# Performance work log

Hardware: AMD Instinct MI355X
Metric: run time of the kernel (lower is better)

## Reference

```python
import jax, jax.numpy as jnp
import numpy as np

B, T, E, H = 4, 2048, 1024, 1024

def setup_inputs() -> dict:
    key = jax.random.key(0)
    k1, k2, k3, k4 = jax.random.split(key, 4)
    inputs = jax.random.normal(k1, (B, T, E), dtype=jnp.float32)
    # Dense(size, use_bias=False) -> weight [emb, size], glorot-ish scale
    Wq = jax.random.normal(k2, (E, H), dtype=jnp.float32) * (1.0 / np.sqrt(E))
    Wk = jax.random.normal(k3, (E, H), dtype=jnp.float32) * (1.0 / np.sqrt(E))
    Wv = jax.random.normal(k4, (E, H), dtype=jnp.float32) * (1.0 / np.sqrt(E))
    return {"inputs": inputs, "Wq": Wq, "Wk": Wk, "Wv": Wv}

def reference(inputs, Wq, Wk, Wv):
    # inputs: [B, T, E]
    _, Tc, Ec = inputs.shape
    q = inputs @ Wq  # [B, T, H]
    k = inputs @ Wk  # [B, T, H]
    v = inputs @ Wv  # [B, T, H]
    # scores scaled by emb_dim**-0.5 (NOT head size) as in the source
    w = jnp.einsum('bih,bjh->bij', q, k) * (Ec ** -0.5)  # [B, T, T]
    tril = jnp.tril(jnp.ones((Tc, Tc), dtype=bool))
    w = jnp.where(tril, w, -jnp.inf)
    # NOTE: source uses softmax over axis=1 (query axis), non-standard but faithful
    w = jax.nn.softmax(w, axis=1)
    # dropout_rate=0.0 -> identity
    out = w @ v  # [B, T, H]
    return out
```

## Files before the change

kernel.cpp:

```cpp
#include <hip/hip_runtime.h>
#include <hip/hip_bf16.h>
#include <stdint.h>


typedef short bf16x8 __attribute__((ext_vector_type(8)));
typedef float f32x4  __attribute__((ext_vector_type(4)));

__device__ __forceinline__ unsigned short f2bf(float f) {
    union { float f; unsigned u; } x; x.f = f;
    unsigned r = x.u + 0x7FFFu + ((x.u >> 16) & 1u);
    return (unsigned short)(r >> 16);
}
__device__ __forceinline__ float bf2f(unsigned short h) {
    union { unsigned u; float f; } x; x.u = ((unsigned)h) << 16;
    return x.f;
}

__global__ __launch_bounds__(256) void cast_kernel(
    const float* __restrict__ in, unsigned short* __restrict__ out, size_t n)
{
    size_t i = ((size_t)blockIdx.x * 256 + threadIdx.x) * 4;
    if (i >= n) return;
    float4 v = *(const float4*)(in + i);
    union { unsigned short h[4]; unsigned long long u; } p;
    p.h[0] = f2bf(v.x); p.h[1] = f2bf(v.y); p.h[2] = f2bf(v.z); p.h[3] = f2bf(v.w);
    *(unsigned long long*)(out + i) = p.u;
}

__global__ __launch_bounds__(256) void transpose_cast_kernel(
    const float* __restrict__ in, unsigned short* __restrict__ out, int R, int C)
{
    __shared__ unsigned short tile[64][65];
    int tx = threadIdx.x & 63, ty = threadIdx.x >> 6;
    int r0 = blockIdx.y * 64, c0 = blockIdx.x * 64;
#pragma unroll
    for (int i = 0; i < 16; ++i) {
        int r = ty + i * 4;
        tile[r][tx] = f2bf(in[(size_t)(r0 + r) * C + c0 + tx]);
    }
    __syncthreads();
#pragma unroll
    for (int i = 0; i < 16; ++i) {
        int c = ty + i * 4;
        out[(size_t)(c0 + c) * R + r0 + tx] = tile[tx][c];
    }
}

template <int MODE>
__global__ __launch_bounds__(256, 3) void gemm_nt(
    const unsigned short* __restrict__ A, const unsigned short* __restrict__ B,
    void* __restrict__ Cout, unsigned short* __restrict__ C2,
    unsigned short* __restrict__ C3, float* __restrict__ fpar,
    int M, int N, int K,
    size_t sAb, size_t sBb, size_t sCb, float scale, int ldt)
{
    int tn, tm, bz = blockIdx.z;
    if (MODE == 4) {
        unsigned id = blockIdx.y * gridDim.x + blockIdx.x;
        unsigned xcd = id & 7, k2 = id >> 3;
        tm = (int)(xcd * 8 + (k2 & 7));
        tn = (int)(k2 >> 3);
    } else if (MODE == 5) {
        int tid = blockIdx.x;
        tm = (int)((sqrtf(8.f * (float)tid + 1.f) - 1.f) * 0.5f);
        while ((tm + 1) * (tm + 2) / 2 <= tid) ++tm;
        while (tm * (tm + 1) / 2 > tid) --tm;
        tn = tid - tm * (tm + 1) / 2;
    } else {
        tn = blockIdx.x; tm = blockIdx.y;
    }
    A += (size_t)bz * sAb;
    B += (size_t)bz * sBb;
    int m0 = tm * 128, n0 = tn * 128;
    int kmax = (MODE == 2) ? (m0 + 128) : K;

    __shared__ unsigned short sAB[2 * 128 * 64];
    char* sAc = (char*)sAB;
    char* sBc = (char*)sAB + 16384;

    unsigned t = threadIdx.x, lane = t & 63, wave = t >> 6;

    unsigned srow = t >> 2;
    unsigned gsw = (t & 3) ^ ((t >> 3) & 3);
    const unsigned short* pA = A + (size_t)(m0 + srow) * K + gsw * 8;
    const unsigned short* pB = B + (size_t)(n0 + srow) * K + gsw * 8;
    const size_t rstep = (size_t)64 * K;
    unsigned ldsOff = t * 16;

    unsigned wm = (wave >> 1) * 64, wn = (wave & 1) * 64;
    unsigned lrow = lane & 15;
    unsigned lk = ((lane >> 4) ^ ((lane >> 1) & 3)) * 8;
    const short* sAs = (const short*)sAB;
    const short* sBs = (const short*)(sAB + 128 * 64);

    f32x4 acc[4][4] = {};

    int4 rA0 = *(const int4*)(pA);
    int4 rA1 = *(const int4*)(pA + rstep);
    int4 rA2 = *(const int4*)(pA + 32);
    int4 rA3 = *(const int4*)(pA + rstep + 32);
    int4 rB0 = *(const int4*)(pB);
    int4 rB1 = *(const int4*)(pB + rstep);
    int4 rB2 = *(const int4*)(pB + 32);
    int4 rB3 = *(const int4*)(pB + rstep + 32);

    for (int k0 = 0; k0 < kmax; k0 += 64) {
        __syncthreads();
        *(int4*)(sAc + ldsOff)         = rA0;
        *(int4*)(sAc + ldsOff + 4096)  = rA1;
        *(int4*)(sAc + ldsOff + 8192)  = rA2;
        *(int4*)(sAc + ldsOff + 12288) = rA3;
        *(int4*)(sBc + ldsOff)         = rB0;
        *(int4*)(sBc + ldsOff + 4096)  = rB1;
        *(int4*)(sBc + ldsOff + 8192)  = rB2;
        *(int4*)(sBc + ldsOff + 12288) = rB3;
        __syncthreads();

        if (k0 + 64 < kmax) {
            pA += 64; pB += 64;
            rA0 = *(const int4*)(pA);
            rA1 = *(const int4*)(pA + rstep);
            rA2 = *(const int4*)(pA + 32);
            rA3 = *(const int4*)(pA + rstep + 32);
            rB0 = *(const int4*)(pB);
            rB1 = *(const int4*)(pB + rstep);
            rB2 = *(const int4*)(pB + 32);
            rB3 = *(const int4*)(pB + rstep + 32);
        }

#pragma unroll
        for (int kk = 0; kk < 2; ++kk) {
            bf16x8 a[4], b[4];
#pragma unroll
            for (int i = 0; i < 4; ++i) {
                a[i] = *(const bf16x8*)(sAs + kk * 4096 + (wm + i * 16 + lrow) * 32 + lk);
                b[i] = *(const bf16x8*)(sBs + kk * 4096 + (wn + i * 16 + lrow) * 32 + lk);
            }
#pragma unroll
            for (int i = 0; i < 4; ++i)
#pragma unroll
                for (int j = 0; j < 4; ++j)
                    acc[i][j] = __builtin_amdgcn_mfma_f32_16x16x32_bf16(
                        a[i], b[j], acc[i][j], 0, 0, 0);
        }
    }

    unsigned col = lane & 15, rq = (lane >> 4) * 4;
    if (MODE == 2) {
        float* C = (float*)Cout + (size_t)bz * sCb;
#pragma unroll
        for (int i = 0; i < 4; ++i)
#pragma unroll
            for (int j = 0; j < 4; ++j)
#pragma unroll
                for (int r = 0; r < 4; ++r)
                    C[(size_t)(m0 + wm + i * 16 + rq + r) * N + n0 + wn + j * 16 + col] =
                        acc[i][j][r];
    } else if (MODE == 5) {
        unsigned short* Ebp = (unsigned short*)Cout + (size_t)bz * sCb;
        float* par = fpar + (size_t)bz * 32 * 2048;
        bool diag = (tm == tn);
        unsigned short* tile = sAB;
        __syncthreads();
#pragma unroll
        for (int jj = 0; jj < 4; ++jj) {
            float csum = 0.f;
            int jl = (int)(wn + jj * 16 + col);
            int jg = n0 + jl;
#pragma unroll
            for (int ii = 0; ii < 4; ++ii) {
#pragma unroll
                for (int r = 0; r < 4; ++r) {
                    int il = (int)(wm + ii * 16 + rq + r);
                    int ig = m0 + il;
                    unsigned short us = 0;
                    if (!diag || ig >= jg)
                        us = f2bf(__expf(acc[ii][jj][r] * scale));
                    tile[il * 128 + jl] = us;
                    csum += bf2f(us);
                }
            }
            csum += __shfl_xor(csum, 16);
            csum += __shfl_xor(csum, 32);
            if (lane < 16) {
                int rh = (m0 + wm) >> 6;
                par[(size_t)rh * 2048 + n0 + wn + jj * 16 + lane] = csum;
            }
        }
        __syncthreads();
        {
            unsigned rr = t >> 4, cc = (t & 15) * 8;
#pragma unroll
            for (int p = 0; p < 8; ++p) {
                int li = (int)(p * 16 + rr);
                int4 v = *(const int4*)(tile + li * 128 + cc);
                *(int4*)(Ebp + (size_t)(m0 + li) * N + n0 + cc) = v;
            }
        }
    } else {
        if (n0 < 2048) {
            unsigned short* C = (n0 < 1024) ? (unsigned short*)Cout : C2;
            int nb = n0 & 1023;
#pragma unroll
            for (int i = 0; i < 4; ++i)
#pragma unroll
                for (int j = 0; j < 4; ++j)
#pragma unroll
                    for (int r = 0; r < 4; ++r)
                        C[(size_t)(m0 + wm + i * 16 + rq + r) * 1024 + nb + wn + j * 16 + col] =
                            f2bf(acc[i][j][r]);
        } else {
            int batch = m0 >> 11, tb = m0 & 2047;
            unsigned short* C = C3 + (size_t)batch * 1024 * 2048;
#pragma unroll
            for (int i = 0; i < 4; ++i)
#pragma unroll
                for (int j = 0; j < 4; ++j) {
                    union { unsigned short h[4]; unsigned long long u; } p;
#pragma unroll
                    for (int r = 0; r < 4; ++r) p.h[r] = f2bf(acc[i][j][r]);
                    int h = (n0 - 2048) + wn + j * 16 + col;
                    int t0 = tb + wm + i * 16 + rq;
                    *(unsigned long long*)(C + (size_t)h * ldt + t0) = p.u;
                }
        }
    }
}

__global__ __launch_bounds__(256) void colsum_inv(
    const float* __restrict__ par, float* __restrict__ Linv, int T)
{
    int b = blockIdx.y;
    int j = blockIdx.x * 256 + threadIdx.x;
    const float* p = par + (size_t)b * 32 * 2048;
    float s = 0.f;
    for (int rh = j >> 6; rh < 32; ++rh) s += p[(size_t)rh * 2048 + j];
    Linv[b * 2048 + j] = 1.0f / s;
}

__global__ __launch_bounds__(256) void scale_v(
    unsigned short* __restrict__ Vt, const float* __restrict__ Linv)
{
    size_t idx = ((size_t)blockIdx.x * 256 + threadIdx.x) * 8;
    int b = (int)(idx >> 21);
    int tt = (int)(idx & 2047);
    bf16x8 v = *(bf16x8*)(Vt + idx);
    const float* L = Linv + b * 2048 + tt;
#pragma unroll
    for (int e = 0; e < 8; ++e)
        v[e] = (short)f2bf(bf2f((unsigned short)v[e]) * L[e]);
    *(bf16x8*)(Vt + idx) = v;
}

extern "C" void kernel_launch(void* const* d_in, const int* in_sizes, int n_in,
                              void* d_out, int out_size, void* d_ws, size_t ws_size,
                              hipStream_t stream)
{
    const int B = 4, T = 2048, E = 1024, H = 1024;
    const int M = B * T;
    const float* X  = (const float*)d_in[0];
    const float* Wq = (const float*)d_in[1];
    const float* Wk = (const float*)d_in[2];
    const float* Wv = (const float*)d_in[3];
    float* out = (float*)d_out;
    char* ws = (char*)d_ws;
    const size_t MB = 1024 * 1024;

    unsigned short* Xb  = (unsigned short*)(ws + 0);
    unsigned short* WqT = (unsigned short*)(ws + 16 * MB);
    unsigned short* WkT = (unsigned short*)(ws + 18 * MB);
    unsigned short* WvT = (unsigned short*)(ws + 20 * MB);
    unsigned short* Qb  = (unsigned short*)(ws + 32 * MB);
    unsigned short* Kb  = (unsigned short*)(ws + 48 * MB);
    unsigned short* Vt  = (unsigned short*)(ws + 64 * MB);
    unsigned short* Eb  = (unsigned short*)(ws + 0);
    float*          Linv = (float*)(ws + 32 * MB);
    float*          par  = (float*)d_out;

    cast_kernel<<<dim3((M * E) / 1024), 256, 0, stream>>>(X, Xb, (size_t)M * E);
    transpose_cast_kernel<<<dim3(H / 64, E / 64), 256, 0, stream>>>(Wq, WqT, E, H);
    transpose_cast_kernel<<<dim3(H / 64, E / 64), 256, 0, stream>>>(Wk, WkT, E, H);
    transpose_cast_kernel<<<dim3(H / 64, E / 64), 256, 0, stream>>>(Wv, WvT, E, H);

    gemm_nt<4><<<dim3(3 * H / 128, M / 128, 1), 256, 0, stream>>>(
        Xb, WqT, Qb, Kb, Vt, nullptr, M, 3 * H, E, 0, 0, 0, 1.f, T);

    gemm_nt<5><<<dim3(136, 1, B), 256, 0, stream>>>(
        Qb, Kb, Eb, nullptr, nullptr, par, T, T, H,
        (size_t)T * H, (size_t)T * H, (size_t)T * T, 0.03125f, T);

    colsum_inv<<<dim3(T / 256, B), 256, 0, stream>>>(par, Linv, T);
    scale_v<<<dim3((B * H * T) / 2048), 256, 0, stream>>>(Vt, Linv);

    gemm_nt<2><<<dim3(H / 128, T / 128, B), 256, 0, stream>>>(
        Eb, Vt, out, nullptr, nullptr, nullptr, T, H, T,
        (size_t)T * T, (size_t)H * T, (size_t)T * H, 1.f, 0);
}
```

Baseline: 251.6 us.

## Fuse prep kernels, fuse colsum with V scaling, remap GEMM block schedules

Merges the X cast and the three weight transpose-casts into one launch, and merges the column-sum/inverse with the V scaling so the inverse stays in shared memory. Block-to-tile mapping changes: the triangular QK^T grid is interleaved so blocks on the same XCD get a spread of tile workloads, and the causal PV GEMM runs as a flattened 1D grid that pairs heavy and light row tiles across batches. The aim is fewer launches and better load balance across XCDs. The cost is more complex index math, and the fused colsum_scale has only 128 blocks, which may underuse the GPU.

Result: faster. 228.4 us (-9.2%).

```diff
diff --git a/kernel.cpp b/kernel.cpp
--- a/kernel.cpp
+++ b/kernel.cpp
@@ -16,33 +16,41 @@
     return x.f;
 }
 
-__global__ __launch_bounds__(256) void cast_kernel(
-    const float* __restrict__ in, unsigned short* __restrict__ out, size_t n)
-{
-    size_t i = ((size_t)blockIdx.x * 256 + threadIdx.x) * 4;
-    if (i >= n) return;
-    float4 v = *(const float4*)(in + i);
-    union { unsigned short h[4]; unsigned long long u; } p;
-    p.h[0] = f2bf(v.x); p.h[1] = f2bf(v.y); p.h[2] = f2bf(v.z); p.h[3] = f2bf(v.w);
-    *(unsigned long long*)(out + i) = p.u;
-}
-
-__global__ __launch_bounds__(256) void transpose_cast_kernel(
-    const float* __restrict__ in, unsigned short* __restrict__ out, int R, int C)
+__global__ __launch_bounds__(256) void prep_kernel(
+    const float* __restrict__ X,
+    const float* __restrict__ Wq, const float* __restrict__ Wk,
+    const float* __restrict__ Wv,
+    unsigned short* __restrict__ Xb, unsigned short* __restrict__ WT)
 {
     __shared__ unsigned short tile[64][65];
-    int tx = threadIdx.x & 63, ty = threadIdx.x >> 6;
-    int r0 = blockIdx.y * 64, c0 = blockIdx.x * 64;
-#pragma unroll
-    for (int i = 0; i < 16; ++i) {
-        int r = ty + i * 4;
-        tile[r][tx] = f2bf(in[(size_t)(r0 + r) * C + c0 + tx]);
-    }
-    __syncthreads();
-#pragma unroll
-    for (int i = 0; i < 16; ++i) {
-        int c = ty + i * 4;
-        out[(size_t)(c0 + c) * R + r0 + tx] = tile[tx][c];
+    unsigned id = blockIdx.x;
+    if (id < 8192) {
+        size_t i = ((size_t)id * 256 + threadIdx.x) * 4;
+        float4 v = *(const float4*)(X + i);
+        union { unsigned short h[4]; unsigned long long u; } p;
+        p.h[0] = f2bf(v.x); p.h[1] = f2bf(v.y);
+        p.h[2] = f2bf(v.z); p.h[3] = f2bf(v.w);
+        *(unsigned long long*)(Xb + i) = p.u;
+    } else {
+        unsigned w = id - 8192;
+        unsigned which = w >> 8;
+        const float* W = (which == 0) ? Wq : (which == 1) ? Wk : Wv;
+        unsigned short* out = WT + (size_t)which * 1024 * 1024;
+        const int R = 1024, C = 1024;
+        unsigned t2 = w & 255;
+        int c0 = (int)(t2 & 15) * 64, r0 = (int)(t2 >> 4) * 64;
+        int tx = threadIdx.x & 63, ty = threadIdx.x >> 6;
+#pragma unroll
+        for (int i = 0; i < 16; ++i) {
+            int r = ty + i * 4;
+            tile[r][tx] = f2bf(W[(size_t)(r0 + r) * C + c0 + tx]);
+        }
+        __syncthreads();
+#pragma unroll
+        for (int i = 0; i < 16; ++i) {
+            int c = ty + i * 4;
+            out[(size_t)(c0 + c) * R + r0 + tx] = tile[tx][c];
+        }
     }
 }
 
@@ -61,13 +69,18 @@
         tm = (int)(xcd * 8 + (k2 & 7));
         tn = (int)(k2 >> 3);
     } else if (MODE == 5) {
-        int tid = blockIdx.x;
+        int bxr = blockIdx.x;
+        int tid = (bxr & 7) * 17 + (bxr >> 3);
         tm = (int)((sqrtf(8.f * (float)tid + 1.f) - 1.f) * 0.5f);
         while ((tm + 1) * (tm + 2) / 2 <= tid) ++tm;
         while (tm * (tm + 1) / 2 > tid) --tm;
         tn = tid - tm * (tm + 1) / 2;
     } else {
-        tn = blockIdx.x; tm = blockIdx.y;
+        unsigned n = blockIdx.x;
+        tn = (int)(n & 7u);
+        unsigned q = n >> 3, half = q >> 5, r = q & 31u;
+        bz = (int)((half ? 2u : 0u) + (r & 1u));
+        tm = half ? (int)(r >> 1) : (int)(15u - (r >> 1));
     }
     A += (size_t)bz * sAb;
     B += (size_t)bz * sBb;
@@ -227,29 +240,32 @@
     }
 }
 
-__global__ __launch_bounds__(256) void colsum_inv(
-    const float* __restrict__ par, float* __restrict__ Linv, int T)
+__global__ __launch_bounds__(256) void colsum_scale(
+    const float* __restrict__ par, unsigned short* __restrict__ Vt)
 {
-    int b = blockIdx.y;
-    int j = blockIdx.x * 256 + threadIdx.x;
-    const float* p = par + (size_t)b * 32 * 2048;
-    float s = 0.f;
-    for (int rh = j >> 6; rh < 32; ++rh) s += p[(size_t)rh * 2048 + j];
-    Linv[b * 2048 + j] = 1.0f / s;
-}
-
-__global__ __launch_bounds__(256) void scale_v(
-    unsigned short* __restrict__ Vt, const float* __restrict__ Linv)
-{
-    size_t idx = ((size_t)blockIdx.x * 256 + threadIdx.x) * 8;
-    int b = (int)(idx >> 21);
-    int tt = (int)(idx & 2047);
-    bf16x8 v = *(bf16x8*)(Vt + idx);
-    const float* L = Linv + b * 2048 + tt;
-#pragma unroll
-    for (int e = 0; e < 8; ++e)
-        v[e] = (short)f2bf(bf2f((unsigned short)v[e]) * L[e]);
-    *(bf16x8*)(Vt + idx) = v;
+    int b = blockIdx.y, t0 = blockIdx.x * 64;
+    __shared__ float Ls[64];
+    int tid = threadIdx.x;
+    if (tid < 64) {
+        int j = t0 + tid;
+        const float* p = par + (size_t)b * 32 * 2048;
+        float s = 0.f;
+        for (int rh = j >> 6; rh < 32; ++rh) s += p[(size_t)rh * 2048 + j];
+        Ls[tid] = 1.0f / s;
+    }
+    __syncthreads();
+    unsigned short* V = Vt + ((size_t)b << 21);
+    int c8 = (tid & 7) * 8;
+#pragma unroll 4
+    for (int hb = 0; hb < 1024; hb += 32) {
+        int h = hb + (tid >> 3);
+        size_t idx = (size_t)h * 2048 + t0 + c8;
+        bf16x8 v = *(bf16x8*)(V + idx);
+#pragma unroll
+        for (int e = 0; e < 8; ++e)
+            v[e] = (short)f2bf(bf2f((unsigned short)v[e]) * Ls[c8 + e]);
+        *(bf16x8*)(V + idx) = v;
+    }
 }
 
 extern "C" void kernel_launch(void* const* d_in, const int* in_sizes, int n_in,
@@ -268,31 +284,24 @@
 
     unsigned short* Xb  = (unsigned short*)(ws + 0);
     unsigned short* WqT = (unsigned short*)(ws + 16 * MB);
-    unsigned short* WkT = (unsigned short*)(ws + 18 * MB);
-    unsigned short* WvT = (unsigned short*)(ws + 20 * MB);
     unsigned short* Qb  = (unsigned short*)(ws + 32 * MB);
     unsigned short* Kb  = (unsigned short*)(ws + 48 * MB);
     unsigned short* Vt  = (unsigned short*)(ws + 64 * MB);
     unsigned short* Eb  = (unsigned short*)(ws + 0);
-    float*          Linv = (float*)(ws + 32 * MB);
     float*          par  = (float*)d_out;
 
-    cast_kernel<<<dim3((M * E) / 1024), 256, 0, stream>>>(X, Xb, (size_t)M * E);
-    transpose_cast_kernel<<<dim3(H / 64, E / 64), 256, 0, stream>>>(Wq, WqT, E, H);
-    transpose_cast_kernel<<<dim3(H / 64, E / 64), 256, 0, stream>>>(Wk, WkT, E, H);
-    transpose_cast_kernel<<<dim3(H / 64, E / 64), 256, 0, stream>>>(Wv, WvT, E, H);
-
-    gemm_nt<4><<<dim3(3 * H / 128, M / 128, 1), 256, 0, stream>>>(
+    prep_kernel<<<dim3(8960), 256, 0, stream>>>(X, Wq, Wk, Wv, Xb, WqT);
+
+    gemm_nt<4><<<dim3(24, 64, 1), 256, 0, stream>>>(
         Xb, WqT, Qb, Kb, Vt, nullptr, M, 3 * H, E, 0, 0, 0, 1.f, T);
 
     gemm_nt<5><<<dim3(136, 1, B), 256, 0, stream>>>(
         Qb, Kb, Eb, nullptr, nullptr, par, T, T, H,
         (size_t)T * H, (size_t)T * H, (size_t)T * T, 0.03125f, T);
 
-    colsum_inv<<<dim3(T / 256, B), 256, 0, stream>>>(par, Linv, T);
-    scale_v<<<dim3((B * H * T) / 2048), 256, 0, stream>>>(Vt, Linv);
-
-    gemm_nt<2><<<dim3(H / 128, T / 128, B), 256, 0, stream>>>(
+    colsum_scale<<<dim3(T / 64, B), 256, 0, stream>>>(par, Vt);
+
+    gemm_nt<2><<<dim3(512, 1, 1), 256, 0, stream>>>(
         Eb, Vt, out, nullptr, nullptr, nullptr, T, H, T,
         (size_t)T * T, (size_t)H * T, (size_t)T * H, 1.f, 0);
 }
```
